# Performance work log

Measured on AMD Instinct MI355X. Metric: run time of the kernel, lower is better.

The kernel has to match this reference:

```python
import itertools
import jax, jax.numpy as jnp
import numpy as np

# ---- JPEG constants (match utils.y_table / utils.c_table) ----
_Y_TABLE = np.array([
    [16, 11, 10, 16, 24, 40, 51, 61],
    [12, 12, 14, 19, 26, 58, 60, 55],
    [14, 13, 16, 24, 40, 57, 69, 56],
    [14, 17, 22, 29, 51, 87, 80, 62],
    [18, 22, 37, 56, 68, 109, 103, 77],
    [24, 35, 55, 64, 81, 104, 113, 92],
    [49, 64, 78, 87, 103, 121, 120, 101],
    [72, 92, 95, 98, 112, 100, 103, 99]], dtype=np.float32)
_C_TABLE = np.full((8, 8), 99, dtype=np.float32)
_C_TABLE[:4, :4] = np.array([[17, 18, 24, 47], [18, 21, 26, 66],
                             [24, 26, 56, 99], [47, 66, 99, 99]], dtype=np.float32)

# RGB -> YCbCr matrix (code defines M then uses M.T via tensordot dims=1)
_YCBCR_M = np.array([[0.299, 0.587, 0.114],
                     [-0.168736, -0.331264, 0.5],
                     [0.5, -0.418688, -0.081312]], dtype=np.float32)
_SHIFT = np.array([0.0, 128.0, 128.0], dtype=np.float32)

_cx = np.cos((2 * np.arange(8)[:, None] + 1) * np.arange(8)[None, :] * np.pi / 16)  # [x,u]
_DCT = np.einsum('xu,yv->xyuv', _cx, _cx).astype(np.float32)
_alpha = np.array([1.0 / np.sqrt(2)] + [1.0] * 7)
_DCT_SCALE = (np.outer(_alpha, _alpha) * 0.25).astype(np.float32)

FACTOR = 1.0
K = 8  # block size


def _block_split(x):
    # x: [B, H, W] -> [B, H*W/64, 8, 8]
    B, H, W = x.shape
    x = x.reshape(B, H // K, K, W // K, K)
    x = jnp.transpose(x, (0, 1, 3, 2, 4))
    return x.reshape(B, -1, K, K)


def _dct_8x8(x):
    # x: [B, N, 8, 8]
    x = x - 128.0
    return jnp.asarray(_DCT_SCALE) * jnp.einsum('bnxy,xyuv->bnuv', x, jnp.asarray(_DCT))


def _avg_pool2(x):
    # 2x2 average pooling, stride 2; x: [B, H, W]
    B, H, W = x.shape
    return x.reshape(B, H // 2, 2, W // 2, 2).mean(axis=(2, 4))


def _compress(image):
    # image: [B, 3, H, W] in [0, 1]
    img = jnp.transpose(image * 255.0, (0, 2, 3, 1))  # [B, H, W, 3]
    ycbcr = jnp.einsum('bhwc,cd->bhwd', img, jnp.asarray(_YCBCR_M.T)) + jnp.asarray(_SHIFT)
    y = ycbcr[..., 0]
    cb = _avg_pool2(ycbcr[..., 1])
    cr = _avg_pool2(ycbcr[..., 2])
    y_q = jnp.round(_dct_8x8(_block_split(y)) / (jnp.asarray(_Y_TABLE) * FACTOR))
    cb_q = jnp.round(_dct_8x8(_block_split(cb)) / (jnp.asarray(_C_TABLE) * FACTOR))
    cr_q = jnp.round(_dct_8x8(_block_split(cr)) / (jnp.asarray(_C_TABLE) * FACTOR))
    return y_q, cb_q, cr_q


def setup_inputs() -> dict:
    key = jax.random.key(0)
    image = jax.random.uniform(key, (32, 3, 512, 512), dtype=jnp.float32)
    return {"image": image}


def reference(image):
    return _compress(image)
```

## Files before the change

### kernel.cpp

```cpp
#include <hip/hip_runtime.h>
#include <cmath>


namespace jc {

constexpr double c1 = 0.98078528040323044912618223613424;
constexpr double c2 = 0.92387953251128675612818318939679;
constexpr double c3 = 0.83146961230254523707878837761791;
constexpr double c4 = 0.70710678118654752440084436210485;
constexpr double c5 = 0.55557023301960222474283081394853;
constexpr double c6 = 0.38268343236508977172845998403040;
constexpr double c7 = 0.19509032201612826784828486847702;
constexpr double alpha0 = 0.70710678118654746171979706919384;

struct Tab {
  float tt[4096];
  float sc[64];
  float yq[64];
  float cq[64];
  constexpr Tab() : tt(), sc(), yq(), cq() {
    const double CX[8][8] = {
      {1.0,  c1,  c2,  c3,  c4,  c5,  c6,  c7},
      {1.0,  c3,  c6, -c7, -c4, -c1, -c2, -c5},
      {1.0,  c5, -c6, -c1, -c4,  c7,  c2,  c3},
      {1.0,  c7, -c2, -c5,  c4,  c3, -c6, -c1},
      {1.0, -c7, -c2,  c5,  c4, -c3, -c6,  c1},
      {1.0, -c5, -c6,  c1, -c4, -c7,  c2, -c3},
      {1.0, -c3,  c6,  c7, -c4,  c1, -c2,  c5},
      {1.0, -c1,  c2, -c3,  c4, -c5,  c6, -c7}};
    for (int i = 0; i < 64; ++i) {
      const int u = i >> 3, v = i & 7;
      for (int j = 0; j < 64; ++j) {
        const int x = j >> 3, y = j & 7;
        tt[j * 64 + i] = (float)(CX[x][u] * CX[y][v]);
      }
      const double au = (u == 0) ? alpha0 : 1.0;
      const double av = (v == 0) ? alpha0 : 1.0;
      sc[i] = (float)((au * av) * 0.25);
    }
    const int YT[64] = {
      16, 11, 10, 16, 24, 40, 51, 61,
      12, 12, 14, 19, 26, 58, 60, 55,
      14, 13, 16, 24, 40, 57, 69, 56,
      14, 17, 22, 29, 51, 87, 80, 62,
      18, 22, 37, 56, 68, 109, 103, 77,
      24, 35, 55, 64, 81, 104, 113, 92,
      49, 64, 78, 87, 103, 121, 120, 101,
      72, 92, 95, 98, 112, 100, 103, 99};
    const int CT[64] = {
      17, 18, 24, 47, 99, 99, 99, 99,
      18, 21, 26, 66, 99, 99, 99, 99,
      24, 26, 56, 99, 99, 99, 99, 99,
      47, 66, 99, 99, 99, 99, 99, 99,
      99, 99, 99, 99, 99, 99, 99, 99,
      99, 99, 99, 99, 99, 99, 99, 99,
      99, 99, 99, 99, 99, 99, 99, 99,
      99, 99, 99, 99, 99, 99, 99, 99};
    for (int i = 0; i < 64; ++i) {
      yq[i] = (float)YT[i];
      cq[i] = (float)CT[i];
    }
  }
};

__device__ constexpr Tab TT;

}

__device__ __forceinline__ float vmul(float a, float b) {
  float r; asm("v_mul_f32 %0, %1, %2" : "=v"(r) : "v"(a), "v"(b)); return r;
}
__device__ __forceinline__ float vadd(float a, float b) {
  float r; asm("v_add_f32 %0, %1, %2" : "=v"(r) : "v"(a), "v"(b)); return r;
}
__device__ __forceinline__ float vsubf(float a, float b) {
  float r; asm("v_sub_f32 %0, %1, %2" : "=v"(r) : "v"(a), "v"(b)); return r;
}

__device__ __forceinline__ float chro_t(float tR, float tG, float tB,
                                        float kR, float kG, float kB) {
  float a = vmul(tR, kR);
  a = vadd(a, vmul(tG, kG));
  a = vadd(a, vmul(tB, kB));
  return vadd(a, 128.0f);
}

__global__ __launch_bounds__(256, 4) void jpeg_kernel(const float* __restrict__ img,
                                                      float* __restrict__ out) {
  __shared__ float Xs[96][68];

  const int wid = blockIdx.x;
  const int t = threadIdx.x;
  const int b = wid >> 6;
  const int r = wid & 63;

  {
    const int yb = t & 63;
    const int q = t >> 6;
    const int by = yb >> 3, bx = yb & 7;
    const int prow = (r >> 3) * 64 + by * 8 + 2 * q;
    const int pcol = (r & 7) * 64 + bx * 8;
    const float* rp = img + (size_t)b * 786432 + (size_t)prow * 512 + pcol;

    float tv[3][2][8];
#pragma unroll
    for (int c = 0; c < 3; ++c) {
#pragma unroll
      for (int rr = 0; rr < 2; ++rr) {
        const float* p0 = rp + c * 262144 + rr * 512;
        const float4 va = *(const float4*)(p0);
        const float4 vb = *(const float4*)(p0 + 4);
        tv[c][rr][0] = vmul(va.x, 255.0f);
        tv[c][rr][1] = vmul(va.y, 255.0f);
        tv[c][rr][2] = vmul(va.z, 255.0f);
        tv[c][rr][3] = vmul(va.w, 255.0f);
        tv[c][rr][4] = vmul(vb.x, 255.0f);
        tv[c][rr][5] = vmul(vb.y, 255.0f);
        tv[c][rr][6] = vmul(vb.z, 255.0f);
        tv[c][rr][7] = vmul(vb.w, 255.0f);
      }
    }
#pragma unroll
    for (int rr = 0; rr < 2; ++rr) {
#pragma unroll
      for (int y = 0; y < 8; ++y) {
        float a = vmul(tv[0][rr][y], 0.299f);
        a = vadd(a, vmul(tv[1][rr][y], 0.587f));
        a = vadd(a, vmul(tv[2][rr][y], 0.114f));
        Xs[yb][16 * q + rr * 8 + y] = vsubf(a, 128.0f);
      }
    }
    const int lcr = 4 * by + q;
#pragma unroll
    for (int pc = 0; pc < 4; ++pc) {
      const int lcc = 4 * bx + pc;
      const int crow = 64 + ((lcr >> 3) * 4 + (lcc >> 3));
      const int cell = (lcr & 7) * 8 + (lcc & 7);
      const int e = 2 * pc, o = 2 * pc + 1;
      {
        const float p00 = chro_t(tv[0][0][e], tv[1][0][e], tv[2][0][e], -0.168736f, -0.331264f, 0.5f);
        const float p01 = chro_t(tv[0][0][o], tv[1][0][o], tv[2][0][o], -0.168736f, -0.331264f, 0.5f);
        const float p10 = chro_t(tv[0][1][e], tv[1][1][e], tv[2][1][e], -0.168736f, -0.331264f, 0.5f);
        const float p11 = chro_t(tv[0][1][o], tv[1][1][o], tv[2][1][o], -0.168736f, -0.331264f, 0.5f);
        const float s = vadd(vadd(vadd(p00, p01), p10), p11);
        Xs[crow][cell] = vsubf(vmul(s, 0.25f), 128.0f);
      }
      {
        const float p00 = chro_t(tv[0][0][e], tv[1][0][e], tv[2][0][e], 0.5f, -0.418688f, -0.081312f);
        const float p01 = chro_t(tv[0][0][o], tv[1][0][o], tv[2][0][o], 0.5f, -0.418688f, -0.081312f);
        const float p10 = chro_t(tv[0][1][e], tv[1][1][e], tv[2][1][e], 0.5f, -0.418688f, -0.081312f);
        const float p11 = chro_t(tv[0][1][o], tv[1][1][o], tv[2][1][o], 0.5f, -0.418688f, -0.081312f);
        const float s = vadd(vadd(vadd(p00, p01), p10), p11);
        Xs[crow + 16][cell] = vsubf(vmul(s, 0.25f), 128.0f);
      }
    }
  }

  const int w = t >> 6;
  const int lane = t & 63;
  float T[64];
#pragma unroll
  for (int j = 0; j < 64; ++j) T[j] = jc::TT.tt[j * 64 + lane];
  const float scv = jc::TT.sc[lane];
  const float yqv = jc::TT.yq[lane];
  const float cqv = jc::TT.cq[lane];

  __syncthreads();

  const int ybase = b * 4096 + (r >> 3) * 512 + (r & 7) * 8;
  const int cbase = b * 1024 + (r >> 3) * 128 + (r & 7) * 4;

  auto emit = [&](int blk, float acc) {
    float qv;
    size_t off;
    if (blk < 64) {
      qv = yqv;
      off = ((size_t)(ybase + (blk >> 3) * 64 + (blk & 7))) << 6;
    } else {
      qv = cqv;
      const int cc = blk & 15;
      off = (size_t)8388608 + (blk >= 80 ? (size_t)2097152 : (size_t)0) +
            (((size_t)(cbase + (cc >> 2) * 32 + (cc & 3))) << 6);
    }
    out[off + lane] = rintf(__fdiv_rn(vmul(scv, acc), qv));
  };

  for (int n = 0; n < 24; n += 2) {
    const int bA = w * 24 + n;
    const int bB = bA + 1;
    float a0 = 0.0f, a1 = 0.0f;
#pragma unroll
    for (int j4 = 0; j4 < 16; ++j4) {
      const float4 xA = *(const float4*)&Xs[bA][j4 * 4];
      const float4 xB = *(const float4*)&Xs[bB][j4 * 4];
      a0 = vadd(a0, vmul(T[4 * j4 + 0], xA.x));
      a1 = vadd(a1, vmul(T[4 * j4 + 0], xB.x));
      a0 = vadd(a0, vmul(T[4 * j4 + 1], xA.y));
      a1 = vadd(a1, vmul(T[4 * j4 + 1], xB.y));
      a0 = vadd(a0, vmul(T[4 * j4 + 2], xA.z));
      a1 = vadd(a1, vmul(T[4 * j4 + 2], xB.z));
      a0 = vadd(a0, vmul(T[4 * j4 + 3], xA.w));
      a1 = vadd(a1, vmul(T[4 * j4 + 3], xB.w));
    }
    emit(bA, a0);
    emit(bB, a1);
  }
}

extern "C" void kernel_launch(void* const* d_in, const int* in_sizes, int n_in,
                              void* d_out, int out_size, void* d_ws, size_t ws_size,
                              hipStream_t stream) {
  (void)in_sizes; (void)n_in; (void)d_ws; (void)ws_size; (void)out_size;
  const float* img = (const float*)d_in[0];
  float* out = (float*)d_out;
  jpeg_kernel<<<dim3(2048), dim3(256), 0, stream>>>(img, out);
}
```

Measured before the change: 185.6 us.

## Assign one 8x8 block per lane, removing LDS staging and using scalar DCT coefficients

Each lane now owns a whole 8x8 block in registers and computes all 64 DCT outputs itself. The coefficients are read as wave-uniform scalar operands from a transposed constant table, so the shared-memory staging buffer and the barrier go away, and outputs are written as float4 per lane. The grid shrinks to 768 blocks, one wave per group of 64 blocks. Each lane now reads 8 consecutive floats per row at strided addresses, which coalesces less well. Parallelism is also much lower, with only 3072 waves and a long serial FMA chain per lane.

```diff
diff --git a/kernel.cpp b/kernel.cpp
--- a/kernel.cpp
+++ b/kernel.cpp
@@ -14,11 +14,11 @@
 constexpr double alpha0 = 0.70710678118654746171979706919384;
 
 struct Tab {
-  float tt[4096];
+  float tr[4096];
   float sc[64];
   float yq[64];
   float cq[64];
-  constexpr Tab() : tt(), sc(), yq(), cq() {
+  constexpr Tab() : tr(), sc(), yq(), cq() {
     const double CX[8][8] = {
       {1.0,  c1,  c2,  c3,  c4,  c5,  c6,  c7},
       {1.0,  c3,  c6, -c7, -c4, -c1, -c2, -c5},
@@ -32,7 +32,7 @@
       const int u = i >> 3, v = i & 7;
       for (int j = 0; j < 64; ++j) {
         const int x = j >> 3, y = j & 7;
-        tt[j * 64 + i] = (float)(CX[x][u] * CX[y][v]);
+        tr[i * 64 + j] = (float)(CX[x][u] * CX[y][v]);
       }
       const double au = (u == 0) ? alpha0 : 1.0;
       const double av = (v == 0) ? alpha0 : 1.0;
@@ -70,6 +70,9 @@
 __device__ __forceinline__ float vmul(float a, float b) {
   float r; asm("v_mul_f32 %0, %1, %2" : "=v"(r) : "v"(a), "v"(b)); return r;
 }
+__device__ __forceinline__ float vmulS(float s, float v) {
+  float r; asm("v_mul_f32 %0, %1, %2" : "=v"(r) : "s"(s), "v"(v)); return r;
+}
 __device__ __forceinline__ float vadd(float a, float b) {
   float r; asm("v_add_f32 %0, %1, %2" : "=v"(r) : "v"(a), "v"(b)); return r;
 }
@@ -85,125 +88,100 @@
   return vadd(a, 128.0f);
 }
 
+__device__ __forceinline__ void ld8(const float* __restrict__ p, float* d) {
+  const float4 a = *(const float4*)(p);
+  const float4 b = *(const float4*)(p + 4);
+  d[0] = vmul(a.x, 255.0f); d[1] = vmul(a.y, 255.0f);
+  d[2] = vmul(a.z, 255.0f); d[3] = vmul(a.w, 255.0f);
+  d[4] = vmul(b.x, 255.0f); d[5] = vmul(b.y, 255.0f);
+  d[6] = vmul(b.z, 255.0f); d[7] = vmul(b.w, 255.0f);
+}
+
 __global__ __launch_bounds__(256, 4) void jpeg_kernel(const float* __restrict__ img,
                                                       float* __restrict__ out) {
-  __shared__ float Xs[96][68];
+  const int t = threadIdx.x;
+  const int lane = t & 63;
+  const int w = __builtin_amdgcn_readfirstlane(t >> 6);
+  const int gw = blockIdx.x * 4 + w;
+  const int im = gw / 96;
+  const int wv = gw - im * 96;
 
-  const int wid = blockIdx.x;
-  const int t = threadIdx.x;
-  const int b = wid >> 6;
-  const int r = wid & 63;
+  const float* base = img + (size_t)im * 786432;
+  float X[64];
+  unsigned obase;
+  bool isY;
 
-  {
-    const int yb = t & 63;
-    const int q = t >> 6;
-    const int by = yb >> 3, bx = yb & 7;
-    const int prow = (r >> 3) * 64 + by * 8 + 2 * q;
-    const int pcol = (r & 7) * 64 + bx * 8;
-    const float* rp = img + (size_t)b * 786432 + (size_t)prow * 512 + pcol;
-
-    float tv[3][2][8];
+  if (wv < 64) {
+    isY = true;
+    const float* rp = base + (wv * 8) * 512 + lane * 8;
 #pragma unroll
-    for (int c = 0; c < 3; ++c) {
+    for (int rr = 0; rr < 8; ++rr) {
+      float tR[8], tG[8], tB[8];
+      ld8(rp + rr * 512, tR);
+      ld8(rp + 262144 + rr * 512, tG);
+      ld8(rp + 524288 + rr * 512, tB);
 #pragma unroll
-      for (int rr = 0; rr < 2; ++rr) {
-        const float* p0 = rp + c * 262144 + rr * 512;
-        const float4 va = *(const float4*)(p0);
-        const float4 vb = *(const float4*)(p0 + 4);
-        tv[c][rr][0] = vmul(va.x, 255.0f);
-        tv[c][rr][1] = vmul(va.y, 255.0f);
-        tv[c][rr][2] = vmul(va.z, 255.0f);
-        tv[c][rr][3] = vmul(va.w, 255.0f);
-        tv[c][rr][4] = vmul(vb.x, 255.0f);
-        tv[c][rr][5] = vmul(vb.y, 255.0f);
-        tv[c][rr][6] = vmul(vb.z, 255.0f);
-        tv[c][rr][7] = vmul(vb.w, 255.0f);
+      for (int y = 0; y < 8; ++y) {
+        float a = vmul(tR[y], 0.299f);
+        a = vadd(a, vmul(tG[y], 0.587f));
+        a = vadd(a, vmul(tB[y], 0.114f));
+        X[rr * 8 + y] = vsubf(a, 128.0f);
       }
     }
+    obase = ((unsigned)(im * 4096 + wv * 64 + lane)) << 6;
+  } else {
+    isY = false;
+    const int cwv = wv - 64;
+    const bool isCb = (cwv < 16);
+    const int m = cwv & 15;
+    const int cy = 2 * m + (lane >> 5);
+    const int cx = lane & 31;
+    const float kR = isCb ? -0.168736f : 0.5f;
+    const float kG = isCb ? -0.331264f : -0.418688f;
+    const float kB = isCb ? 0.5f : -0.081312f;
+    const float* rp = base + (cy * 16) * 512 + cx * 16;
 #pragma unroll
-    for (int rr = 0; rr < 2; ++rr) {
+    for (int q = 0; q < 8; ++q) {
 #pragma unroll
-      for (int y = 0; y < 8; ++y) {
-        float a = vmul(tv[0][rr][y], 0.299f);
-        a = vadd(a, vmul(tv[1][rr][y], 0.587f));
-        a = vadd(a, vmul(tv[2][rr][y], 0.114f));
-        Xs[yb][16 * q + rr * 8 + y] = vsubf(a, 128.0f);
+      for (int h = 0; h < 2; ++h) {
+        const float* p0 = rp + (2 * q) * 512 + 8 * h;
+        float tR0[8], tR1[8], tG0[8], tG1[8], tB0[8], tB1[8];
+        ld8(p0, tR0);           ld8(p0 + 512, tR1);
+        ld8(p0 + 262144, tG0);  ld8(p0 + 262144 + 512, tG1);
+        ld8(p0 + 524288, tB0);  ld8(p0 + 524288 + 512, tB1);
+#pragma unroll
+        for (int c2 = 0; c2 < 4; ++c2) {
+          const int e = 2 * c2, o = e + 1;
+          const float p00 = chro_t(tR0[e], tG0[e], tB0[e], kR, kG, kB);
+          const float p01 = chro_t(tR0[o], tG0[o], tB0[o], kR, kG, kB);
+          const float p10 = chro_t(tR1[e], tG1[e], tB1[e], kR, kG, kB);
+          const float p11 = chro_t(tR1[o], tG1[o], tB1[o], kR, kG, kB);
+          const float s = vadd(vadd(vadd(p00, p01), p10), p11);
+          X[q * 8 + h * 4 + c2] = vsubf(vmul(s, 0.25f), 128.0f);
+        }
       }
     }
-    const int lcr = 4 * by + q;
-#pragma unroll
-    for (int pc = 0; pc < 4; ++pc) {
-      const int lcc = 4 * bx + pc;
-      const int crow = 64 + ((lcr >> 3) * 4 + (lcc >> 3));
-      const int cell = (lcr & 7) * 8 + (lcc & 7);
-      const int e = 2 * pc, o = 2 * pc + 1;
-      {
-        const float p00 = chro_t(tv[0][0][e], tv[1][0][e], tv[2][0][e], -0.168736f, -0.331264f, 0.5f);
-        const float p01 = chro_t(tv[0][0][o], tv[1][0][o], tv[2][0][o], -0.168736f, -0.331264f, 0.5f);
-        const float p10 = chro_t(tv[0][1][e], tv[1][1][e], tv[2][1][e], -0.168736f, -0.331264f, 0.5f);
-        const float p11 = chro_t(tv[0][1][o], tv[1][1][o], tv[2][1][o], -0.168736f, -0.331264f, 0.5f);
-        const float s = vadd(vadd(vadd(p00, p01), p10), p11);
-        Xs[crow][cell] = vsubf(vmul(s, 0.25f), 128.0f);
-      }
-      {
-        const float p00 = chro_t(tv[0][0][e], tv[1][0][e], tv[2][0][e], 0.5f, -0.418688f, -0.081312f);
-        const float p01 = chro_t(tv[0][0][o], tv[1][0][o], tv[2][0][o], 0.5f, -0.418688f, -0.081312f);
-        const float p10 = chro_t(tv[0][1][e], tv[1][1][e], tv[2][1][e], 0.5f, -0.418688f, -0.081312f);
-        const float p11 = chro_t(tv[0][1][o], tv[1][1][o], tv[2][1][o], 0.5f, -0.418688f, -0.081312f);
-        const float s = vadd(vadd(vadd(p00, p01), p10), p11);
-        Xs[crow + 16][cell] = vsubf(vmul(s, 0.25f), 128.0f);
-      }
-    }
+    obase = 8388608u + (isCb ? 0u : 2097152u) +
+            (((unsigned)(im * 1024 + m * 64 + lane)) << 6);
   }
 
-  const int w = t >> 6;
-  const int lane = t & 63;
-  float T[64];
+  const float* __restrict__ qt = isY ? jc::TT.yq : jc::TT.cq;
+  float* op = out + obase;
+#pragma unroll 1
+  for (int i0 = 0; i0 < 64; i0 += 4) {
+    float ov[4];
 #pragma unroll
-  for (int j = 0; j < 64; ++j) T[j] = jc::TT.tt[j * 64 + lane];
-  const float scv = jc::TT.sc[lane];
-  const float yqv = jc::TT.yq[lane];
-  const float cqv = jc::TT.cq[lane];
-
-  __syncthreads();
-
-  const int ybase = b * 4096 + (r >> 3) * 512 + (r & 7) * 8;
-  const int cbase = b * 1024 + (r >> 3) * 128 + (r & 7) * 4;
-
-  auto emit = [&](int blk, float acc) {
-    float qv;
-    size_t off;
-    if (blk < 64) {
-      qv = yqv;
-      off = ((size_t)(ybase + (blk >> 3) * 64 + (blk & 7))) << 6;
-    } else {
-      qv = cqv;
-      const int cc = blk & 15;
-      off = (size_t)8388608 + (blk >= 80 ? (size_t)2097152 : (size_t)0) +
-            (((size_t)(cbase + (cc >> 2) * 32 + (cc & 3))) << 6);
+    for (int ii = 0; ii < 4; ++ii) {
+      const int i = i0 + ii;
+      const float* __restrict__ trow = jc::TT.tr + i * 64;
+      float acc = 0.0f;
+#pragma unroll
+      for (int j = 0; j < 64; ++j)
+        acc = vadd(acc, vmulS(trow[j], X[j]));
+      ov[ii] = rintf(__fdiv_rn(vmulS(jc::TT.sc[i], acc), qt[i]));
     }
-    out[off + lane] = rintf(__fdiv_rn(vmul(scv, acc), qv));
-  };
-
-  for (int n = 0; n < 24; n += 2) {
-    const int bA = w * 24 + n;
-    const int bB = bA + 1;
-    float a0 = 0.0f, a1 = 0.0f;
-#pragma unroll
-    for (int j4 = 0; j4 < 16; ++j4) {
-      const float4 xA = *(const float4*)&Xs[bA][j4 * 4];
-      const float4 xB = *(const float4*)&Xs[bB][j4 * 4];
-      a0 = vadd(a0, vmul(T[4 * j4 + 0], xA.x));
-      a1 = vadd(a1, vmul(T[4 * j4 + 0], xB.x));
-      a0 = vadd(a0, vmul(T[4 * j4 + 1], xA.y));
-      a1 = vadd(a1, vmul(T[4 * j4 + 1], xB.y));
-      a0 = vadd(a0, vmul(T[4 * j4 + 2], xA.z));
-      a1 = vadd(a1, vmul(T[4 * j4 + 2], xB.z));
-      a0 = vadd(a0, vmul(T[4 * j4 + 3], xA.w));
-      a1 = vadd(a1, vmul(T[4 * j4 + 3], xB.w));
-    }
-    emit(bA, a0);
-    emit(bB, a1);
+    float4 v4; v4.x = ov[0]; v4.y = ov[1]; v4.z = ov[2]; v4.w = ov[3];
+    *(float4*)(op + i0) = v4;
   }
 }
 
@@ -213,5 +191,5 @@
   (void)in_sizes; (void)n_in; (void)d_ws; (void)ws_size; (void)out_size;
   const float* img = (const float*)d_in[0];
   float* out = (float*)d_out;
-  jpeg_kernel<<<dim3(2048), dim3(256), 0, stream>>>(img, out);
+  jpeg_kernel<<<dim3(768), dim3(256), 0, stream>>>(img, out);
 }
```

After: 334.8 us. 80.4% more time.

## Map one DCT block per lane with scalar coefficient table and staged stores

Applied to the files above, without the earlier changes.

The DCT stage is remapped so that each lane holds one 8x8 block's 64 inputs in registers, loaded once from LDS. It then iterates over output coefficients, reading the basis table from constant memory as scalar operands, which removes the repeated per-coefficient LDS reads and the 64-register basis column per lane. Results are staged back through LDS and written to global memory as coalesced float4 stores. The cost is that the chroma waves leave half their lanes idle, so total issued ALU work rises, and register pressure from the 64 held inputs may limit occupancy.

```diff
diff --git a/kernel.cpp b/kernel.cpp
--- a/kernel.cpp
+++ b/kernel.cpp
@@ -14,11 +14,11 @@
 constexpr double alpha0 = 0.70710678118654746171979706919384;
 
 struct Tab {
-  float tt[4096];
+  float tr[4096];
   float sc[64];
   float yq[64];
   float cq[64];
-  constexpr Tab() : tt(), sc(), yq(), cq() {
+  constexpr Tab() : tr(), sc(), yq(), cq() {
     const double CX[8][8] = {
       {1.0,  c1,  c2,  c3,  c4,  c5,  c6,  c7},
       {1.0,  c3,  c6, -c7, -c4, -c1, -c2, -c5},
@@ -32,7 +32,7 @@
       const int u = i >> 3, v = i & 7;
       for (int j = 0; j < 64; ++j) {
         const int x = j >> 3, y = j & 7;
-        tt[j * 64 + i] = (float)(CX[x][u] * CX[y][v]);
+        tr[i * 64 + j] = (float)(CX[x][u] * CX[y][v]);
       }
       const double au = (u == 0) ? alpha0 : 1.0;
       const double av = (v == 0) ? alpha0 : 1.0;
@@ -63,12 +63,15 @@
   }
 };
 
-__device__ constexpr Tab TT;
-
-}
+}
+
+__constant__ jc::Tab TT;
 
 __device__ __forceinline__ float vmul(float a, float b) {
   float r; asm("v_mul_f32 %0, %1, %2" : "=v"(r) : "v"(a), "v"(b)); return r;
+}
+__device__ __forceinline__ float vmulS(float s, float v) {
+  float r; asm("v_mul_f32 %0, %1, %2" : "=v"(r) : "s"(s), "v"(v)); return r;
 }
 __device__ __forceinline__ float vadd(float a, float b) {
   float r; asm("v_add_f32 %0, %1, %2" : "=v"(r) : "v"(a), "v"(b)); return r;
@@ -85,12 +88,39 @@
   return vadd(a, 128.0f);
 }
 
-__global__ __launch_bounds__(256, 4) void jpeg_kernel(const float* __restrict__ img,
-                                                      float* __restrict__ out) {
-  __shared__ float Xs[96][68];
-
+#define REP64(F) F(0) F(1) F(2) F(3) F(4) F(5) F(6) F(7) \
+  F(8) F(9) F(10) F(11) F(12) F(13) F(14) F(15) \
+  F(16) F(17) F(18) F(19) F(20) F(21) F(22) F(23) \
+  F(24) F(25) F(26) F(27) F(28) F(29) F(30) F(31) \
+  F(32) F(33) F(34) F(35) F(36) F(37) F(38) F(39) \
+  F(40) F(41) F(42) F(43) F(44) F(45) F(46) F(47) \
+  F(48) F(49) F(50) F(51) F(52) F(53) F(54) F(55) \
+  F(56) F(57) F(58) F(59) F(60) F(61) F(62) F(63)
+
+#define DECLX(j) float X##j;
+
+#define LDX(k, XA, XB, XC, XD) do { \
+  const float4 v_ = *(const float4*)&LDSbuf[blk * 68 + 4 * (k)]; \
+  XA = v_.x; XB = v_.y; XC = v_.z; XD = v_.w; \
+} while (0)
+
+#define MACJ(j) acc = vadd(acc, vmulS(trow[j], X##j));
+#define DCT1(iexpr, dest) do { \
+  const int i_ = (iexpr); \
+  const float* trow = TT.tr + i_ * 64; \
+  float acc = 0.0f; \
+  REP64(MACJ) \
+  dest = rintf(__fdiv_rn(vmulS(TT.sc[i_], acc), qt[i_])); \
+} while (0)
+
+__global__ __launch_bounds__(256, 4)
+void jpeg_kernel(const float* __restrict__ img, float* __restrict__ out) {
+  __shared__ float LDSbuf[96 * 68];
+
+  const int t = threadIdx.x;
+  const int lane = t & 63;
+  const int w = __builtin_amdgcn_readfirstlane(t >> 6);
   const int wid = blockIdx.x;
-  const int t = threadIdx.x;
   const int b = wid >> 6;
   const int r = wid & 63;
 
@@ -127,7 +157,7 @@
         float a = vmul(tv[0][rr][y], 0.299f);
         a = vadd(a, vmul(tv[1][rr][y], 0.587f));
         a = vadd(a, vmul(tv[2][rr][y], 0.114f));
-        Xs[yb][16 * q + rr * 8 + y] = vsubf(a, 128.0f);
+        LDSbuf[yb * 68 + 16 * q + rr * 8 + y] = vsubf(a, 128.0f);
       }
     }
     const int lcr = 4 * by + q;
@@ -143,7 +173,7 @@
         const float p10 = chro_t(tv[0][1][e], tv[1][1][e], tv[2][1][e], -0.168736f, -0.331264f, 0.5f);
         const float p11 = chro_t(tv[0][1][o], tv[1][1][o], tv[2][1][o], -0.168736f, -0.331264f, 0.5f);
         const float s = vadd(vadd(vadd(p00, p01), p10), p11);
-        Xs[crow][cell] = vsubf(vmul(s, 0.25f), 128.0f);
+        LDSbuf[crow * 68 + cell] = vsubf(vmul(s, 0.25f), 128.0f);
       }
       {
         const float p00 = chro_t(tv[0][0][e], tv[1][0][e], tv[2][0][e], 0.5f, -0.418688f, -0.081312f);
@@ -151,59 +181,83 @@
         const float p10 = chro_t(tv[0][1][e], tv[1][1][e], tv[2][1][e], 0.5f, -0.418688f, -0.081312f);
         const float p11 = chro_t(tv[0][1][o], tv[1][1][o], tv[2][1][o], 0.5f, -0.418688f, -0.081312f);
         const float s = vadd(vadd(vadd(p00, p01), p10), p11);
-        Xs[crow + 16][cell] = vsubf(vmul(s, 0.25f), 128.0f);
-      }
-    }
-  }
-
-  const int w = t >> 6;
-  const int lane = t & 63;
-  float T[64];
-#pragma unroll
-  for (int j = 0; j < 64; ++j) T[j] = jc::TT.tt[j * 64 + lane];
-  const float scv = jc::TT.sc[lane];
-  const float yqv = jc::TT.yq[lane];
-  const float cqv = jc::TT.cq[lane];
+        LDSbuf[(crow + 16) * 68 + cell] = vsubf(vmul(s, 0.25f), 128.0f);
+      }
+    }
+  }
+
+  const int ibase = (w & 1) * 32;
+  const bool chro = (w >= 2);
+  const bool active = (!chro) || (lane < 32);
+  const int blk = chro ? (64 + (lane & 31)) : lane;
+  const float* qt = chro ? TT.cq : TT.yq;
+
+  REP64(DECLX)
+
+  __syncthreads();
+
+  if (active) {
+    LDX(0,  X0,  X1,  X2,  X3);
+    LDX(1,  X4,  X5,  X6,  X7);
+    LDX(2,  X8,  X9,  X10, X11);
+    LDX(3,  X12, X13, X14, X15);
+    LDX(4,  X16, X17, X18, X19);
+    LDX(5,  X20, X21, X22, X23);
+    LDX(6,  X24, X25, X26, X27);
+    LDX(7,  X28, X29, X30, X31);
+    LDX(8,  X32, X33, X34, X35);
+    LDX(9,  X36, X37, X38, X39);
+    LDX(10, X40, X41, X42, X43);
+    LDX(11, X44, X45, X46, X47);
+    LDX(12, X48, X49, X50, X51);
+    LDX(13, X52, X53, X54, X55);
+    LDX(14, X56, X57, X58, X59);
+    LDX(15, X60, X61, X62, X63);
+  }
 
   __syncthreads();
 
   const int ybase = b * 4096 + (r >> 3) * 512 + (r & 7) * 8;
   const int cbase = b * 1024 + (r >> 3) * 128 + (r & 7) * 4;
 
-  auto emit = [&](int blk, float acc) {
-    float qv;
-    size_t off;
-    if (blk < 64) {
-      qv = yqv;
-      off = ((size_t)(ybase + (blk >> 3) * 64 + (blk & 7))) << 6;
+#pragma unroll 1
+  for (int f = 0; f < 2; ++f) {
+    if (active) {
+#pragma unroll 1
+      for (int g = 0; g < 4; ++g) {
+        const int ib = ibase + f * 16 + g * 4;
+        float o0, o1, o2, o3;
+        DCT1(ib + 0, o0);
+        DCT1(ib + 1, o1);
+        DCT1(ib + 2, o2);
+        DCT1(ib + 3, o3);
+        float4 v4; v4.x = o0; v4.y = o1; v4.z = o2; v4.w = o3;
+        *(float4*)&LDSbuf[(w * 64 + lane) * 20 + g * 4] = v4;
+      }
+    }
+    const int co = ibase + f * 16;
+    if (!chro) {
+#pragma unroll
+      for (int k = 0; k < 4; ++k) {
+        const int B = k * 16 + (lane >> 2);
+        const int e0 = (lane & 3) * 4;
+        const float4 vv = *(const float4*)&LDSbuf[(w * 64 + B) * 20 + e0];
+        const unsigned ob = (unsigned)(ybase + (B >> 3) * 64 + (B & 7));
+        *(float4*)&out[(ob << 6) + (unsigned)(co + e0)] = vv;
+      }
     } else {
-      qv = cqv;
-      const int cc = blk & 15;
-      off = (size_t)8388608 + (blk >= 80 ? (size_t)2097152 : (size_t)0) +
-            (((size_t)(cbase + (cc >> 2) * 32 + (cc & 3))) << 6);
-    }
-    out[off + lane] = rintf(__fdiv_rn(vmul(scv, acc), qv));
-  };
-
-  for (int n = 0; n < 24; n += 2) {
-    const int bA = w * 24 + n;
-    const int bB = bA + 1;
-    float a0 = 0.0f, a1 = 0.0f;
-#pragma unroll
-    for (int j4 = 0; j4 < 16; ++j4) {
-      const float4 xA = *(const float4*)&Xs[bA][j4 * 4];
-      const float4 xB = *(const float4*)&Xs[bB][j4 * 4];
-      a0 = vadd(a0, vmul(T[4 * j4 + 0], xA.x));
-      a1 = vadd(a1, vmul(T[4 * j4 + 0], xB.x));
-      a0 = vadd(a0, vmul(T[4 * j4 + 1], xA.y));
-      a1 = vadd(a1, vmul(T[4 * j4 + 1], xB.y));
-      a0 = vadd(a0, vmul(T[4 * j4 + 2], xA.z));
-      a1 = vadd(a1, vmul(T[4 * j4 + 2], xB.z));
-      a0 = vadd(a0, vmul(T[4 * j4 + 3], xA.w));
-      a1 = vadd(a1, vmul(T[4 * j4 + 3], xB.w));
-    }
-    emit(bA, a0);
-    emit(bB, a1);
+#pragma unroll
+      for (int k = 0; k < 2; ++k) {
+        const int idx = k * 64 + lane;
+        const int B = idx >> 2;
+        const int e0 = (idx & 3) * 4;
+        const float4 vv = *(const float4*)&LDSbuf[(w * 64 + B) * 20 + e0];
+        const int cc = B & 15;
+        const unsigned ob = 8388608u + (B >= 16 ? 2097152u : 0u) +
+            (((unsigned)(cbase + (cc >> 2) * 32 + (cc & 3))) << 6);
+        *(float4*)&out[ob + (unsigned)(co + e0)] = vv;
+      }
+    }
   }
 }
 
```

New measurement: 308.0 us. +66.0%, slower.
